# Optimization experiments

Hardware: AMD Instinct MI355X
Metric: run time of the kernel (lower is better)

Reference implementation:

```python
import jax, jax.numpy as jnp
import numpy as np

H = 12        # num_attention_heads
A = 16        # agent_num
C = 768       # hidden_size


def setup_inputs() -> dict:
    key = jax.random.key(0)
    ks = jax.random.split(key, 16)
    B, N = 8, 4096
    std = 0.02
    return {
        "s1_hidden_states": jax.random.normal(ks[0], (B, N, C), jnp.float32),
        "s2_hidden_states": jax.random.normal(ks[1], (B, N, C), jnp.float32),
        "Wq": jax.random.normal(ks[2], (C, C), jnp.float32) * std,
        "bq": jnp.zeros((C,), jnp.float32),
        "Wk": jax.random.normal(ks[3], (C, C), jnp.float32) * std,
        "bk": jnp.zeros((C,), jnp.float32),
        "Wv": jax.random.normal(ks[4], (C, C), jnp.float32) * std,
        "bv": jnp.zeros((C,), jnp.float32),
        "an_bias": jax.random.normal(ks[5], (H, A, 7, 7), jnp.float32) * std,
        "na_bias": jax.random.normal(ks[6], (H, A, 7, 7), jnp.float32) * std,
        "ah_bias": jax.random.normal(ks[7], (1, H, A, A, 1), jnp.float32) * std,
        "aw_bias": jax.random.normal(ks[8], (1, H, A, 1, A), jnp.float32) * std,
        "ha_bias": jax.random.normal(ks[9], (1, H, A, 1, A), jnp.float32) * std,
        "wa_bias": jax.random.normal(ks[10], (1, H, 1, A, A), jnp.float32) * std,
    }


def reference(s1_hidden_states, s2_hidden_states, Wq, bq, Wk, bk, Wv, bv,
              an_bias, na_bias, ah_bias, aw_bias, ha_bias, wa_bias):
    b, n, c = s1_hidden_states.shape
    m = s2_hidden_states.shape[1]
    hd = c // H
    scale = hd ** -0.5

    q = s1_hidden_states @ Wq.T + bq            # (b, n, c)
    k = s2_hidden_states @ Wk.T + bk            # (b, m, c)
    v = s2_hidden_states @ Wv.T + bv            # (b, m, c)

    # AdaptiveAvgPool1d(A) with n % A == 0 -> uniform chunk mean
    agent = q.reshape(b, A, n // A, c).mean(axis=2)  # (b, A, c)

    def heads(x):
        return x.reshape(b, -1, H, hd).transpose(0, 2, 1, 3)

    qh, kh, vh = heads(q), heads(k), heads(v)        # (b,H,·,hd)
    ah = heads(agent)                                # (b,H,A,hd)

    # stage 1: agent -> keys.  bias is constant per (h, a) row.
    pb1 = jax.image.resize(an_bias, (H, A, A, A), method='bilinear').reshape(1, H, A, A * A)
    pb2 = (ah_bias + aw_bias).reshape(1, H, A, A * A)
    pb = (pb1 + pb2).mean(axis=-1)                   # (1, H, A)
    agent_attn = jnp.einsum('bhad,bhmd->bham', ah * scale, kh) + pb[:, :, :, None]
    agent_attn = jax.nn.softmax(agent_attn, axis=-1)
    agent_v = jnp.einsum('bham,bhmd->bhad', agent_attn, vh)  # (b,H,A,hd)

    # stage 2: queries -> agents.
    ab1 = jax.image.resize(na_bias, (H, A, A, A), method='bilinear') \
            .reshape(1, H, A, A * A).transpose(0, 1, 3, 2)   # (1,H,A*A,A)
    ab2 = (ha_bias + wa_bias).reshape(1, H, A * A, A)
    ab = (ab1 + ab2).mean(axis=-2)                   # (1, H, A)
    q_attn = jnp.einsum('bhnd,bhad->bhna', qh * scale, ah) + ab[:, :, None, :]
    q_attn = jax.nn.softmax(q_attn, axis=-1)
    x = jnp.einsum('bhna,bhad->bhnd', q_attn, agent_v)  # (b,H,n,hd)
    return x.transpose(0, 2, 1, 3).reshape(b, n, c)
```

## Files before the change

kernel.cpp:

```cpp
#include <hip/hip_runtime.h>
#include <cstdint>
#include <cstddef>

typedef unsigned short ushort_t;
typedef unsigned int uint;

typedef __attribute__((ext_vector_type(8))) short short8;
typedef __attribute__((ext_vector_type(4))) float floatx4;

#define CDIM 768

__device__ __forceinline__ float bfu(ushort_t u) {
    return __uint_as_float(((uint)u) << 16);
}
__device__ __forceinline__ void bf2(uint u, float& lo, float& hi) {
    lo = __uint_as_float(u << 16);
    hi = __uint_as_float(u & 0xffff0000u);
}
__device__ __forceinline__ ushort_t f2bfu(float f) {
    uint u = __float_as_uint(f);
    u += 0x7fffu + ((u >> 16) & 1u);
    return (ushort_t)(u >> 16);
}
__device__ __forceinline__ uint pack2(float a, float b) {
    return (uint)f2bfu(a) | ((uint)f2bfu(b) << 16);
}
__device__ __forceinline__ uint cvt2(float lo, float hi) {
    uint r;
    asm("v_cvt_pk_bf16_f32 %0, %1, %2" : "=v"(r) : "v"(lo), "v"(hi));
    return r;
}
__device__ __forceinline__ short8 mk8(uint a, uint b, uint c, uint d) {
    union { uint4 u; short8 s; } x;
    x.u = (uint4){a, b, c, d};
    return x.s;
}
__device__ __forceinline__ void gload_lds16(const void* g, void* l) {
    __builtin_amdgcn_global_load_lds(
        (__attribute__((address_space(1))) void*)(uintptr_t)g,
        (__attribute__((address_space(3))) void*)l, 16, 0, 0);
}

__global__ __launch_bounds__(256) void prep(
    const float* __restrict__ Wq, const float* __restrict__ Wk,
    const float* __restrict__ Wv, const float* __restrict__ bq,
    const float* __restrict__ na, const float* __restrict__ ha,
    const float* __restrict__ wa,
    ushort_t* __restrict__ wb, float* __restrict__ agent, float* __restrict__ ab)
{
    const int bid = blockIdx.x;
    if (bid < 864) {
        const int m = bid / 288;
        const float* src = (m == 0) ? Wq : (m == 1 ? Wk : Wv);
        ushort_t* dst = wb + (size_t)m * 589824;
        const int i = ((bid % 288) * 256 + threadIdx.x) * 8;
        const float4 f0 = *(const float4*)(src + i);
        const float4 f1 = *(const float4*)(src + i + 4);
        uint4 u;
        u.x = pack2(f0.x, f0.y);
        u.y = pack2(f0.z, f0.w);
        u.z = pack2(f1.x, f1.y);
        u.w = pack2(f1.z, f1.w);
        *(uint4*)(dst + i) = u;
    } else if (bid < 960) {
        const int bh = bid - 864;
        const int h = bh % 12;
        for (int i = threadIdx.x; i < 1024; i += 256)
            agent[(size_t)bh * 1024 + i] = bq[h * 64 + (i & 63)];
    } else {
        const int t = threadIdx.x;
        if (t >= 192) return;
        const int h = t >> 4, a = t & 15;
        const float cw[7] = {2.25f, 2.34375f, 2.28125f, 2.25f, 2.28125f, 2.34375f, 2.25f};
        float acc = 0.f;
        const float* nb = na + (h * 16 + a) * 49;
        for (int i = 0; i < 7; ++i)
            for (int j = 0; j < 7; ++j)
                acc += cw[i] * cw[j] * nb[i * 7 + j];
        acc *= (1.0f / 256.0f);
        float s = 0.f;
        for (int p = 0; p < 16; ++p)
            s += ha[(h * 16 + p) * 16 + a] + wa[(h * 16 + p) * 16 + a];
        ab[t] = acc + s * (1.0f / 16.0f);
    }
}

__global__ __launch_bounds__(256) void cvt_a(
    const float* __restrict__ s1, const float* __restrict__ s2,
    ushort_t* __restrict__ ab)
{
    const int m = blockIdx.y;
    const float* src = (m == 0) ? s1 : s2;
    ushort_t* dst = ab + (size_t)m * 25165824;
    const size_t i = ((size_t)blockIdx.x * 256 + threadIdx.x) * 8;
    const float4 f0 = *(const float4*)(src + i);
    const float4 f1 = *(const float4*)(src + i + 4);
    uint4 u;
    u.x = pack2(f0.x, f0.y);
    u.y = pack2(f0.z, f0.w);
    u.z = pack2(f1.x, f1.y);
    u.w = pack2(f1.z, f1.w);
    *(uint4*)(dst + i) = u;
}

__global__ __launch_bounds__(256, 2) void gemm_qkv(
    const ushort_t* __restrict__ ab, const ushort_t* __restrict__ wb,
    const float* __restrict__ bq, const float* __restrict__ bk, const float* __restrict__ bv,
    ushort_t* __restrict__ qo, ushort_t* __restrict__ ko, ushort_t* __restrict__ vo,
    float* __restrict__ agent)
{
    const int z = blockIdx.z;
    const ushort_t* A     = ab + (size_t)(z != 0) * 25165824;
    const ushort_t* W     = wb + (size_t)z * 589824;
    const float* bias     = (z == 0) ? bq : (z == 1 ? bk : bv);
    ushort_t* out         = (z == 0) ? qo : (z == 1 ? ko : vo);

    __shared__ ushort_t lds[17408];
    ushort_t* At = lds;
    ushort_t* Wt = lds + 8192;

    const int tid  = threadIdx.x;
    const int wave = tid >> 6;
    const int lane = tid & 63;
    const int wm = wave >> 1, wn = wave & 1;

    const int id   = blockIdx.x + (blockIdx.y << 8);
    const int id2  = (id & 7) * 192 + (id >> 3);
    const int row0 = (id2 / 6) * 128;
    const int col0 = (id2 % 6) * 128;

    const int sro = lane >> 3;
    const int sch = ((lane & 7) ^ sro) * 8;
    const ushort_t* gaBase = A + (size_t)(row0 + wave * 32 + sro) * CDIM + sch;
    const ushort_t* gwBase = W + (size_t)(col0 + wave * 32 + sro) * CDIM + sch;

    floatx4 acc[4][4];
    #pragma unroll
    for (int i = 0; i < 4; ++i)
        #pragma unroll
        for (int j = 0; j < 4; ++j)
            acc[i][j] = (floatx4){0.f, 0.f, 0.f, 0.f};

    const int q4 = lane >> 4, r16 = lane & 15;

    for (int kt = 0; kt < CDIM; kt += 64) {
        __syncthreads();
        #pragma unroll
        for (int i = 0; i < 4; ++i) {
            gload_lds16(gaBase + (size_t)i * 8 * CDIM + kt, &At[(wave * 32 + i * 8) * 64]);
            gload_lds16(gwBase + (size_t)i * 8 * CDIM + kt, &Wt[(wave * 32 + i * 8) * 64]);
        }
        __syncthreads();
        #pragma unroll
        for (int ks = 0; ks < 2; ++ks) {
            short8 af[4], bfr[4];
            #pragma unroll
            for (int mt = 0; mt < 4; ++mt) {
                const int row = wm * 64 + mt * 16 + r16;
                const int ch  = (ks * 4 + q4) ^ (row & 7);
                af[mt] = *(const short8*)&At[row * 64 + ch * 8];
            }
            #pragma unroll
            for (int nt = 0; nt < 4; ++nt) {
                const int row = wn * 64 + nt * 16 + r16;
                const int ch  = (ks * 4 + q4) ^ (row & 7);
                bfr[nt] = *(const short8*)&Wt[row * 64 + ch * 8];
            }
            #pragma unroll
            for (int mt = 0; mt < 4; ++mt)
                #pragma unroll
                for (int nt = 0; nt < 4; ++nt)
                    acc[mt][nt] = __builtin_amdgcn_mfma_f32_16x16x32_bf16(
                        af[mt], bfr[nt], acc[mt][nt], 0, 0, 0);
        }
    }

    __syncthreads();
    const int b = row0 >> 12;
    const int m_base = row0 & 4095;
    #pragma unroll
    for (int nt = 0; nt < 4; ++nt) {
        const int coll = wn * 64 + nt * 16 + r16;
        const float bb = bias[col0 + coll];
        float psum = 0.f;
        #pragma unroll
        for (int mt = 0; mt < 4; ++mt) {
            const int rowl = wm * 64 + mt * 16 + q4 * 4;
            #pragma unroll
            for (int r = 0; r < 4; ++r) {
                lds[(rowl + r) * 136 + coll] = f2bfu(acc[mt][nt][r] + bb);
                psum += acc[mt][nt][r];
            }
        }
        if (z == 0) {
            psum += __shfl_xor(psum, 16);
            psum += __shfl_xor(psum, 32);
            if (q4 == 0) {
                const int h = (col0 + coll) >> 6, d = (col0 + coll) & 63;
                atomicAdd(&agent[(size_t)(b * 12 + h) * 1024 + (m_base >> 8) * 64 + d],
                          psum * (1.0f / 256.0f));
            }
        }
    }
    __syncthreads();
    #pragma unroll
    for (int it = 0; it < 8; ++it) {
        const int task  = it * 256 + tid;
        const int chunk = task & 7;
        const int rh    = task >> 3;
        const int rowl  = rh >> 1, hl = rh & 1;
        const uint4 v = *(const uint4*)&lds[rowl * 136 + hl * 64 + chunk * 8];
        ushort_t* op = out + ((size_t)(b * 12 + (col0 >> 6) + hl) * 4096
                              + m_base + rowl) * 64 + chunk * 8;
        *(uint4*)op = v;
    }
}

__global__ __launch_bounds__(512) void stage1(
    const ushort_t* __restrict__ k_hm, const ushort_t* __restrict__ v_hm,
    const float* __restrict__ agent, float* __restrict__ Sp, float* __restrict__ avp)
{
    const int bh = blockIdx.x, z = blockIdx.y;
    const int tid = threadIdx.x;
    const int lane = tid & 63;
    const int w = tid >> 6;
    const int g = lane >> 4;
    const int t = lane & 15;
    __shared__ ushort_t E2[256 * 20];

    short8 ahA[2], ahE[2];
    #pragma unroll
    for (int k0 = 0; k0 < 2; ++k0) {
        const float* p = agent + (size_t)bh * 1024 + t * 64 + k0 * 32 + g * 8;
        const float4 f0 = *(const float4*)p;
        const float4 f1 = *(const float4*)(p + 4);
        const float v[8] = {f0.x, f0.y, f0.z, f0.w, f1.x, f1.y, f1.z, f1.w};
        uint u[4], e[4];
        #pragma unroll
        for (int j = 0; j < 4; ++j) {
            const float a0 = v[2*j] * 0.125f, a1 = v[2*j+1] * 0.125f;
            u[j] = cvt2(a0, a1);
            float b0, b1; bf2(u[j], b0, b1);
            e[j] = cvt2(a0 - b0, a1 - b1);
        }
        ahA[k0] = mk8(u[0], u[1], u[2], u[3]);
        ahE[k0] = mk8(e[0], e[1], e[2], e[3]);
    }

    const int m0 = z * 256;
    const ushort_t* kb = k_hm + ((size_t)bh * 4096 + m0) * 64;

    #pragma unroll
    for (int ti = 0; ti < 2; ++ti) {
        const int row = w * 32 + ti * 16 + t;
        const ushort_t* kp = kb + (size_t)row * 64 + g * 8;
        const short8 kB0 = *(const short8*)(kp);
        const short8 kB1 = *(const short8*)(kp + 32);
        floatx4 sc = {0.f, 0.f, 0.f, 0.f};
        sc = __builtin_amdgcn_mfma_f32_16x16x32_bf16(ahA[0], kB0, sc, 0, 0, 0);
        sc = __builtin_amdgcn_mfma_f32_16x16x32_bf16(ahA[1], kB1, sc, 0, 0, 0);
        sc = __builtin_amdgcn_mfma_f32_16x16x32_bf16(ahE[0], kB0, sc, 0, 0, 0);
        sc = __builtin_amdgcn_mfma_f32_16x16x32_bf16(ahE[1], kB1, sc, 0, 0, 0);
        const uint P0 = pack2(__expf(sc[0]), __expf(sc[1]));
        const uint P1 = pack2(__expf(sc[2]), __expf(sc[3]));
        *(uint2*)&E2[(size_t)row * 20 + g * 4] = make_uint2(P0, P1);
    }
    __syncthreads();

    const int gg = (tid >> 6) & 3;
    const int half = tid >> 8;
    const int ls = lane & 31;
    const int mseg = lane >> 5;
    const int d0 = ls * 2;
    const int mb = half * 128 + mseg * 64;
    const ushort_t* vb = v_hm + ((size_t)bh * 4096 + m0 + mb) * 64 + d0;
    float ac[4][2];
    float ss[4];
    #pragma unroll
    for (int a = 0; a < 4; ++a) { ac[a][0] = 0.f; ac[a][1] = 0.f; ss[a] = 0.f; }
    for (int ml = 0; ml < 64; ++ml) {
        const uint vv = *(const uint*)(vb + (size_t)ml * 64);
        float v0, v1;
        bf2(vv, v0, v1);
        const uint2 ee = *(const uint2*)&E2[(size_t)(mb + ml) * 20 + gg * 4];
        float e0, e1, e2, e3;
        bf2(ee.x, e0, e1);
        bf2(ee.y, e2, e3);
        ac[0][0] += e0 * v0; ac[0][1] += e0 * v1; ss[0] += e0;
        ac[1][0] += e1 * v0; ac[1][1] += e1 * v1; ss[1] += e1;
        ac[2][0] += e2 * v0; ac[2][1] += e2 * v1; ss[2] += e2;
        ac[3][0] += e3 * v0; ac[3][1] += e3 * v1; ss[3] += e3;
    }
    #pragma unroll
    for (int a = 0; a < 4; ++a) {
        ac[a][0] += __shfl_xor(ac[a][0], 32);
        ac[a][1] += __shfl_xor(ac[a][1], 32);
        ss[a]    += __shfl_xor(ss[a], 32);
    }
    const int z2 = z * 2 + half;
    if (mseg == 0) {
        float* avz = avp + (size_t)(z2 * 96 + bh) * 1024;
        #pragma unroll
        for (int a = 0; a < 4; ++a)
            *(float2*)&avz[(gg * 4 + a) * 64 + d0] = make_float2(ac[a][0], ac[a][1]);
        if (ls == 0) {
            #pragma unroll
            for (int a = 0; a < 4; ++a)
                Sp[((size_t)bh * 16 + gg * 4 + a) * 32 + z2] = ss[a];
        }
    }
}

__global__ __launch_bounds__(256) void stage2(
    const ushort_t* __restrict__ q_hm, const float* __restrict__ avp,
    const float* __restrict__ Sp, const float* __restrict__ agent,
    const float* __restrict__ ab, float* __restrict__ out)
{
    const int nb = blockIdx.x;
    const int bh = blockIdx.y;
    const int b = bh / 12, h = bh % 12;
    const int tid = threadIdx.x;
    const int g = (tid >> 4) & 3;
    const int t = tid & 15;
    const int w = tid >> 6;
    __shared__ float avn[1024];

    {
        const int i4 = tid * 4;
        const int a = i4 >> 6;
        floatx4 num = {0.f, 0.f, 0.f, 0.f};
        #pragma unroll
        for (int zz = 0; zz < 32; ++zz)
            num += *(const floatx4*)&avp[(size_t)(zz * 96 + bh) * 1024 + i4];
        const float* sp = Sp + ((size_t)bh * 16 + a) * 32;
        floatx4 dv = {0.f, 0.f, 0.f, 0.f};
        #pragma unroll
        for (int j = 0; j < 8; ++j)
            dv += *(const floatx4*)(sp + j * 4);
        const float r = 1.0f / (dv[0] + dv[1] + dv[2] + dv[3]);
        *(floatx4*)&avn[i4] = num * r;
    }
    __syncthreads();

    short8 ahA[2], ahE[2];
    #pragma unroll
    for (int k0 = 0; k0 < 2; ++k0) {
        const float* p = agent + (size_t)bh * 1024 + t * 64 + k0 * 32 + g * 8;
        const float4 f0 = *(const float4*)p;
        const float4 f1 = *(const float4*)(p + 4);
        const float v[8] = {f0.x, f0.y, f0.z, f0.w, f1.x, f1.y, f1.z, f1.w};
        uint u[4], e[4];
        #pragma unroll
        for (int j = 0; j < 4; ++j) {
            const float a0 = v[2*j] * 0.125f, a1 = v[2*j+1] * 0.125f;
            u[j] = cvt2(a0, a1);
            float b0, b1; bf2(u[j], b0, b1);
            e[j] = cvt2(a0 - b0, a1 - b1);
        }
        ahA[k0] = mk8(u[0], u[1], u[2], u[3]);
        ahE[k0] = mk8(e[0], e[1], e[2], e[3]);
    }

    short8 avf[4], ave[4];
    #pragma unroll
    for (int dt = 0; dt < 4; ++dt) {
        uint u[4] = {0, 0, 0, 0}, e[4] = {0, 0, 0, 0};
        if (g < 2) {
            #pragma unroll
            for (int j = 0; j < 4; ++j) {
                const float a0 = avn[(8*g + 2*j)     * 64 + dt * 16 + t];
                const float a1 = avn[(8*g + 2*j + 1) * 64 + dt * 16 + t];
                u[j] = cvt2(a0, a1);
                float b0, b1; bf2(u[j], b0, b1);
                e[j] = cvt2(a0 - b0, a1 - b1);
            }
        }
        avf[dt] = mk8(u[0], u[1], u[2], u[3]);
        ave[dt] = mk8(e[0], e[1], e[2], e[3]);
    }

    float abv[4];
    #pragma unroll
    for (int r = 0; r < 4; ++r) abv[r] = ab[h * 16 + 4 * g + r];

    const int src0 = (t + 32 * g) & 63;
    const int src1 = (src0 + 16) & 63;
    const int n0 = nb * 256 + w * 64;
    const ushort_t* qb = q_hm + ((size_t)bh * 4096 + n0) * 64;
    float* ob = out + ((size_t)b * 4096 + n0) * CDIM + h * 64;

    #pragma unroll
    for (int ti = 0; ti < 4; ++ti) {
        const ushort_t* qp = qb + (size_t)(ti * 16 + t) * 64 + g * 8;
        const short8 qB0 = *(const short8*)(qp);
        const short8 qB1 = *(const short8*)(qp + 32);

        floatx4 sc = {0.f, 0.f, 0.f, 0.f};
        sc = __builtin_amdgcn_mfma_f32_16x16x32_bf16(ahA[0], qB0, sc, 0, 0, 0);
        sc = __builtin_amdgcn_mfma_f32_16x16x32_bf16(ahA[1], qB1, sc, 0, 0, 0);
        sc = __builtin_amdgcn_mfma_f32_16x16x32_bf16(ahE[0], qB0, sc, 0, 0, 0);
        sc = __builtin_amdgcn_mfma_f32_16x16x32_bf16(ahE[1], qB1, sc, 0, 0, 0);

        const float e0 = __expf(sc[0] + abv[0]);
        const float e1 = __expf(sc[1] + abv[1]);
        const float e2 = __expf(sc[2] + abv[2]);
        const float e3 = __expf(sc[3] + abv[3]);
        float s = e0 + e1 + e2 + e3;
        s += __shfl_xor(s, 16);
        s += __shfl_xor(s, 32);
        const float rs = 1.0f / s;
        const float p0 = e0 * rs, p1 = e1 * rs, p2 = e2 * rs, p3 = e3 * rs;

        const uint P0 = cvt2(p0, p1), P1 = cvt2(p2, p3);
        float q0, q1, q2, q3;
        bf2(P0, q0, q1); bf2(P1, q2, q3);
        const uint E0 = cvt2(p0 - q0, p1 - q1), E1 = cvt2(p2 - q2, p3 - q3);

        uint w0 = __shfl(P0, src0), w1 = __shfl(P1, src0);
        uint w2 = __shfl(P0, src1), w3 = __shfl(P1, src1);
        uint x0 = __shfl(E0, src0), x1 = __shfl(E1, src0);
        uint x2 = __shfl(E0, src1), x3 = __shfl(E1, src1);
        if (g >= 2) { w0 = w1 = w2 = w3 = 0; x0 = x1 = x2 = x3 = 0; }
        const short8 pf = mk8(w0, w1, w2, w3);
        const short8 pe = mk8(x0, x1, x2, x3);

        float* op = ob + (size_t)(ti * 16 + t) * CDIM + 4 * g;
        #pragma unroll
        for (int dt = 0; dt < 4; ++dt) {
            floatx4 od = {0.f, 0.f, 0.f, 0.f};
            od = __builtin_amdgcn_mfma_f32_16x16x32_bf16(avf[dt], pf, od, 0, 0, 0);
            od = __builtin_amdgcn_mfma_f32_16x16x32_bf16(avf[dt], pe, od, 0, 0, 0);
            od = __builtin_amdgcn_mfma_f32_16x16x32_bf16(ave[dt], pf, od, 0, 0, 0);
            *(floatx4*)(op + dt * 16) = od;
        }
    }
}

extern "C" void kernel_launch(void* const* d_in, const int* in_sizes, int n_in,
                              void* d_out, int out_size, void* d_ws, size_t ws_size,
                              hipStream_t stream) {
    (void)in_sizes; (void)n_in; (void)out_size; (void)ws_size;
    const float* s1 = (const float*)d_in[0];
    const float* s2 = (const float*)d_in[1];
    const float* Wq = (const float*)d_in[2];
    const float* bq = (const float*)d_in[3];
    const float* Wk = (const float*)d_in[4];
    const float* bk = (const float*)d_in[5];
    const float* Wv = (const float*)d_in[6];
    const float* bv = (const float*)d_in[7];
    const float* na = (const float*)d_in[9];
    const float* ha = (const float*)d_in[12];
    const float* wa = (const float*)d_in[13];
    float* out = (float*)d_out;

    char* ws = (char*)d_ws;
    ushort_t* q_hm = (ushort_t*)(ws);
    ushort_t* k_hm = (ushort_t*)(ws + 50331648);
    ushort_t* v_hm = (ushort_t*)(ws + 100663296);
    float* agent   = (float*)(ws + 150994944);
    float* Sp      = (float*)(ws + 151388160);
    float* ab      = (float*)(ws + 151584768);
    ushort_t* wb   = (ushort_t*)(ws + 151585536);
    ushort_t* abuf = (ushort_t*)(ws + 155124480);
    float* avp     = (float*)(ws + 155124480);

    prep     <<<dim3(961),       256, 0, stream>>>(Wq, Wk, Wv, bq, na, ha, wa,
                                                   wb, agent, ab);
    cvt_a    <<<dim3(12288, 2),  256, 0, stream>>>(s1, s2, abuf);
    gemm_qkv <<<dim3(256, 6, 3), 256, 0, stream>>>(abuf, wb, bq, bk, bv,
                                                   q_hm, k_hm, v_hm, agent);
    stage1   <<<dim3(96, 16),    512, 0, stream>>>(k_hm, v_hm, agent, Sp, avp);
    stage2   <<<dim3(16, 96),    256, 0, stream>>>(q_hm, avp, Sp, agent, ab, out);
}
```

Before: 268.5 us.

## Merge input and weight conversion kernels; hoist agent-value reduction into its own kernel

Combines the separate prep and activation-conversion kernels into a single cvt_all launch, removing one kernel launch and its tail. It also moves the 32-way partial-sum reduction of agent values out of stage2, where each of the 16 blocks per head recomputed it, into a small redu kernel that writes a normalized buffer once. Stage2 then only copies that buffer into shared memory. The cost is one extra launch and a global round trip for the reduced buffer.

```diff
diff --git a/kernel.cpp b/kernel.cpp
--- a/kernel.cpp
+++ b/kernel.cpp
@@ -41,19 +41,22 @@
         (__attribute__((address_space(3))) void*)l, 16, 0, 0);
 }
 
-__global__ __launch_bounds__(256) void prep(
+__global__ __launch_bounds__(256) void cvt_all(
+    const float* __restrict__ s1, const float* __restrict__ s2,
     const float* __restrict__ Wq, const float* __restrict__ Wk,
     const float* __restrict__ Wv, const float* __restrict__ bq,
     const float* __restrict__ na, const float* __restrict__ ha,
     const float* __restrict__ wa,
-    ushort_t* __restrict__ wb, float* __restrict__ agent, float* __restrict__ ab)
+    ushort_t* __restrict__ abuf, ushort_t* __restrict__ wb,
+    float* __restrict__ agent, float* __restrict__ ab)
 {
     const int bid = blockIdx.x;
-    if (bid < 864) {
-        const int m = bid / 288;
-        const float* src = (m == 0) ? Wq : (m == 1 ? Wk : Wv);
-        ushort_t* dst = wb + (size_t)m * 589824;
-        const int i = ((bid % 288) * 256 + threadIdx.x) * 8;
+    if (bid < 24576) {
+        const int m = (bid >= 12288);
+        const int bx = bid - m * 12288;
+        const float* src = (m == 0) ? s1 : s2;
+        ushort_t* dst = abuf + (size_t)m * 25165824;
+        const size_t i = ((size_t)bx * 256 + threadIdx.x) * 8;
         const float4 f0 = *(const float4*)(src + i);
         const float4 f1 = *(const float4*)(src + i + 4);
         uint4 u;
@@ -62,8 +65,22 @@
         u.z = pack2(f1.x, f1.y);
         u.w = pack2(f1.z, f1.w);
         *(uint4*)(dst + i) = u;
-    } else if (bid < 960) {
-        const int bh = bid - 864;
+    } else if (bid < 25440) {
+        const int wid = bid - 24576;
+        const int m = wid / 288;
+        const float* src = (m == 0) ? Wq : (m == 1 ? Wk : Wv);
+        ushort_t* dst = wb + (size_t)m * 589824;
+        const int i = ((wid % 288) * 256 + threadIdx.x) * 8;
+        const float4 f0 = *(const float4*)(src + i);
+        const float4 f1 = *(const float4*)(src + i + 4);
+        uint4 u;
+        u.x = pack2(f0.x, f0.y);
+        u.y = pack2(f0.z, f0.w);
+        u.z = pack2(f1.x, f1.y);
+        u.w = pack2(f1.z, f1.w);
+        *(uint4*)(dst + i) = u;
+    } else if (bid < 25536) {
+        const int bh = bid - 25440;
         const int h = bh % 12;
         for (int i = threadIdx.x; i < 1024; i += 256)
             agent[(size_t)bh * 1024 + i] = bq[h * 64 + (i & 63)];
@@ -85,24 +102,6 @@
     }
 }
 
-__global__ __launch_bounds__(256) void cvt_a(
-    const float* __restrict__ s1, const float* __restrict__ s2,
-    ushort_t* __restrict__ ab)
-{
-    const int m = blockIdx.y;
-    const float* src = (m == 0) ? s1 : s2;
-    ushort_t* dst = ab + (size_t)m * 25165824;
-    const size_t i = ((size_t)blockIdx.x * 256 + threadIdx.x) * 8;
-    const float4 f0 = *(const float4*)(src + i);
-    const float4 f1 = *(const float4*)(src + i + 4);
-    uint4 u;
-    u.x = pack2(f0.x, f0.y);
-    u.y = pack2(f0.z, f0.w);
-    u.z = pack2(f1.x, f1.y);
-    u.w = pack2(f1.z, f1.w);
-    *(uint4*)(dst + i) = u;
-}
-
 __global__ __launch_bounds__(256, 2) void gemm_qkv(
     const ushort_t* __restrict__ ab, const ushort_t* __restrict__ wb,
     const float* __restrict__ bq, const float* __restrict__ bk, const float* __restrict__ bv,
@@ -311,10 +310,31 @@
     }
 }
 
+__global__ __launch_bounds__(256) void redu(
+    const float* __restrict__ avp, const float* __restrict__ Sp,
+    float* __restrict__ avn_g)
+{
+    const int bh = blockIdx.x;
+    const int tid = threadIdx.x;
+    const int i4 = tid * 4;
+    const int a = i4 >> 6;
+    floatx4 num = {0.f, 0.f, 0.f, 0.f};
+    #pragma unroll
+    for (int zz = 0; zz < 32; ++zz)
+        num += *(const floatx4*)&avp[(size_t)(zz * 96 + bh) * 1024 + i4];
+    const float* sp = Sp + ((size_t)bh * 16 + a) * 32;
+    floatx4 dv = {0.f, 0.f, 0.f, 0.f};
+    #pragma unroll
+    for (int j = 0; j < 8; ++j)
+        dv += *(const floatx4*)(sp + j * 4);
+    const float r = 1.0f / (dv[0] + dv[1] + dv[2] + dv[3]);
+    *(floatx4*)&avn_g[(size_t)bh * 1024 + i4] = num * r;
+}
+
 __global__ __launch_bounds__(256) void stage2(
-    const ushort_t* __restrict__ q_hm, const float* __restrict__ avp,
-    const float* __restrict__ Sp, const float* __restrict__ agent,
-    const float* __restrict__ ab, float* __restrict__ out)
+    const ushort_t* __restrict__ q_hm, const float* __restrict__ avn_g,
+    const float* __restrict__ agent, const float* __restrict__ ab,
+    float* __restrict__ out)
 {
     const int nb = blockIdx.x;
     const int bh = blockIdx.y;
@@ -327,18 +347,7 @@
 
     {
         const int i4 = tid * 4;
-        const int a = i4 >> 6;
-        floatx4 num = {0.f, 0.f, 0.f, 0.f};
-        #pragma unroll
-        for (int zz = 0; zz < 32; ++zz)
-            num += *(const floatx4*)&avp[(size_t)(zz * 96 + bh) * 1024 + i4];
-        const float* sp = Sp + ((size_t)bh * 16 + a) * 32;
-        floatx4 dv = {0.f, 0.f, 0.f, 0.f};
-        #pragma unroll
-        for (int j = 0; j < 8; ++j)
-            dv += *(const floatx4*)(sp + j * 4);
-        const float r = 1.0f / (dv[0] + dv[1] + dv[2] + dv[3]);
-        *(floatx4*)&avn[i4] = num * r;
+        *(floatx4*)&avn[i4] = *(const floatx4*)&avn_g[(size_t)bh * 1024 + i4];
     }
     __syncthreads();
 
@@ -460,15 +469,16 @@
     float* agent   = (float*)(ws + 150994944);
     float* Sp      = (float*)(ws + 151388160);
     float* ab      = (float*)(ws + 151584768);
-    ushort_t* wb   = (ushort_t*)(ws + 151585536);
-    ushort_t* abuf = (ushort_t*)(ws + 155124480);
-    float* avp     = (float*)(ws + 155124480);
-
-    prep     <<<dim3(961),       256, 0, stream>>>(Wq, Wk, Wv, bq, na, ha, wa,
-                                                   wb, agent, ab);
-    cvt_a    <<<dim3(12288, 2),  256, 0, stream>>>(s1, s2, abuf);
+    float* avn_g   = (float*)(ws + 151585536);
+    ushort_t* wb   = (ushort_t*)(ws + 151978752);
+    ushort_t* abuf = (ushort_t*)(ws + 155517696);
+    float* avp     = (float*)(ws + 155517696);
+
+    cvt_all  <<<dim3(25537),     256, 0, stream>>>(s1, s2, Wq, Wk, Wv, bq,
+                                                   na, ha, wa, abuf, wb, agent, ab);
     gemm_qkv <<<dim3(256, 6, 3), 256, 0, stream>>>(abuf, wb, bq, bk, bv,
                                                    q_hm, k_hm, v_hm, agent);
     stage1   <<<dim3(96, 16),    512, 0, stream>>>(k_hm, v_hm, agent, Sp, avp);
-    stage2   <<<dim3(16, 96),    256, 0, stream>>>(q_hm, avp, Sp, agent, ab, out);
-}
+    redu     <<<dim3(96),        256, 0, stream>>>(avp, Sp, avn_g);
+    stage2   <<<dim3(16, 96),    256, 0, stream>>>(q_hm, avn_g, agent, ab, out);
+}
```

New measurement: 263.0 us (median of 2 runs). -2.1%, faster.
